# Performance work log

Hardware: AMD Instinct MI355X
Metric: run time of the kernel (lower is better)

Reference implementation:

```python
import jax, jax.numpy as jnp
import numpy as np

N = 100000      # nodes
D_IN = 512      # in_size
D_OUT = 512     # out_size
E = 200000      # edges per etype
EPS = 1e-5      # LayerNorm eps


def setup_inputs() -> dict:
    key = jax.random.key(0)
    ks = jax.random.split(key, 10)
    scale = 1.0 / np.sqrt(D_IN)
    inp = {
        "x": jax.random.normal(ks[0], (N, D_IN), jnp.float32),
        "W0": jax.random.normal(ks[1], (D_OUT, D_IN), jnp.float32) * scale,
        "W1": jax.random.normal(ks[2], (D_OUT, D_IN), jnp.float32) * scale,
        "W2": jax.random.normal(ks[3], (D_OUT, D_IN), jnp.float32) * scale,
        "gamma": jnp.ones((D_OUT,), jnp.float32),
        "beta": jnp.zeros((D_OUT,), jnp.float32),
        "src0": jax.random.randint(ks[4], (E,), 0, N, jnp.int32),
        "dst0": jax.random.randint(ks[5], (E,), 0, N, jnp.int32),
        "src1": jax.random.randint(ks[6], (E,), 0, N, jnp.int32),
        "dst1": jax.random.randint(ks[7], (E,), 0, N, jnp.int32),
        "src2": jax.random.randint(ks[8], (E,), 0, N, jnp.int32),
        "dst2": jax.random.randint(ks[9], (E,), 0, N, jnp.int32),
    }
    return inp


def _segment_mean(msgs, dst, n):
    # per-dst-node mean; 0 for nodes with no incoming edges (DGL fn.mean semantics)
    s = jax.ops.segment_sum(msgs, dst, num_segments=n)
    c = jax.ops.segment_sum(jnp.ones((msgs.shape[0],), msgs.dtype), dst, num_segments=n)
    return s / jnp.maximum(c, 1.0)[:, None]


def reference(x, W0, W1, W2, gamma, beta, src0, dst0, src1, dst1, src2, dst2):
    # relation-specific linear transforms, averaged over etypes sharing the src ntype
    h = (x @ W0.T + x @ W1.T + x @ W2.T) / 3.0            # [N, D_OUT]
    # per-etype copy_u / mean aggregation
    a0 = _segment_mean(h[src0], dst0, N)
    a1 = _segment_mean(h[src1], dst1, N)
    a2 = _segment_mean(h[src2], dst2, N)
    # cross-etype 'mean' reducer
    h_agg = (a0 + a1 + a2) / 3.0
    # LayerNorm(ReLU(h_agg))
    a = jax.nn.relu(h_agg)
    mu = jnp.mean(a, axis=-1, keepdims=True)
    var = jnp.mean(jnp.square(a - mu), axis=-1, keepdims=True)
    return (a - mu) * jax.lax.rsqrt(var + EPS) * gamma + beta
```

## Files before the change

### kernel.cpp

```cpp
#include <hip/hip_runtime.h>
#include <hip/hip_bf16.h>
#include <cstdint>
#include <cstddef>

#define N_NODES 100000
#define DIM 512
#define NE 200000
#define NBLK 391

typedef __attribute__((ext_vector_type(4))) float floatx4;
typedef __attribute__((ext_vector_type(8))) short shortx8;

__device__ __forceinline__ unsigned short f2bf(float f) {
    union { float f; uint32_t u; } v; v.f = f;
    uint32_t r = v.u + 0x7fff + ((v.u >> 16) & 1);
    return (unsigned short)(r >> 16);
}

__device__ __forceinline__ float bf2f(unsigned short h) {
    union { uint32_t u; float f; } v; v.u = ((uint32_t)h) << 16;
    return v.f;
}

__device__ __forceinline__ shortx8 cvt8(const float4 a, const float4 b) {
    union { __hip_bfloat162 h2[4]; shortx8 s8; } u;
    u.h2[0] = __float22bfloat162_rn(make_float2(a.x, a.y));
    u.h2[1] = __float22bfloat162_rn(make_float2(a.z, a.w));
    u.h2[2] = __float22bfloat162_rn(make_float2(b.x, b.y));
    u.h2[3] = __float22bfloat162_rn(make_float2(b.z, b.w));
    return u.s8;
}

__device__ __forceinline__ void load_lds16(const void* g, void* l) {
    __builtin_amdgcn_global_load_lds(
        (const __attribute__((address_space(1))) uint32_t*)g,
        (__attribute__((address_space(3))) uint32_t*)l, 16, 0, 0);
}

__global__ __launch_bounds__(256) void combine_w_kernel(
    const float* __restrict__ W0, const float* __restrict__ W1,
    const float* __restrict__ W2, unsigned short* __restrict__ Wc) {
    int i = blockIdx.x * 256 + threadIdx.x;
    Wc[i] = f2bf((W0[i] + W1[i] + W2[i]) * (1.0f / 3.0f));
}

__global__ __launch_bounds__(256) void count_kernel(
    const int* __restrict__ d0, const int* __restrict__ d1,
    const int* __restrict__ d2, int* __restrict__ cnt) {
    int t = blockIdx.x * 256 + threadIdx.x;
    if (t >= 3 * NE) return;
    int e = t / NE;
    int i = t - e * NE;
    const int* dp = (e == 0) ? d0 : (e == 1) ? d1 : d2;
    atomicAdd(&cnt[e * N_NODES + dp[i]], 1);
}

__global__ __launch_bounds__(256) void scan1_kernel(
    const int* __restrict__ cnt, int* __restrict__ bsum) {
    int t = threadIdx.x;
    int n = blockIdx.x * 256 + t;
    int rl = 0;
    if (n < N_NODES) rl = cnt[n] + cnt[N_NODES + n] + cnt[2 * N_NODES + n];
    int v = rl;
    #pragma unroll
    for (int off = 32; off > 0; off >>= 1) v += __shfl_xor(v, off);
    __shared__ int ws_[4];
    if ((t & 63) == 0) ws_[t >> 6] = v;
    __syncthreads();
    if (t == 0) bsum[blockIdx.x] = ws_[0] + ws_[1] + ws_[2] + ws_[3];
}

__global__ __launch_bounds__(512) void scan2_kernel(
    const int* __restrict__ bsum, int* __restrict__ boff) {
    __shared__ int sh[512];
    int t = threadIdx.x;
    int v = (t < NBLK) ? bsum[t] : 0;
    sh[t] = v;
    __syncthreads();
    #pragma unroll
    for (int off = 1; off < 512; off <<= 1) {
        int add = (t >= off) ? sh[t - off] : 0;
        __syncthreads();
        sh[t] += add;
        __syncthreads();
    }
    if (t < NBLK) boff[t] = sh[t] - v;
}

__global__ __launch_bounds__(256) void scan3_kernel(
    const int* __restrict__ cnt, const int* __restrict__ boff,
    int* __restrict__ row_start, int* __restrict__ cursor) {
    __shared__ int sh[256];
    int t = threadIdx.x;
    int n = blockIdx.x * 256 + t;
    int rl = 0;
    if (n < N_NODES) rl = cnt[n] + cnt[N_NODES + n] + cnt[2 * N_NODES + n];
    sh[t] = rl;
    __syncthreads();
    #pragma unroll
    for (int off = 1; off < 256; off <<= 1) {
        int add = (t >= off) ? sh[t - off] : 0;
        __syncthreads();
        sh[t] += add;
        __syncthreads();
    }
    if (n < N_NODES) {
        int excl = sh[t] - rl + boff[blockIdx.x];
        row_start[n] = excl;
        cursor[n] = excl;
    }
}

__global__ __launch_bounds__(256) void bin_kernel(
    const int* __restrict__ s0, const int* __restrict__ d0,
    const int* __restrict__ s1, const int* __restrict__ d1,
    const int* __restrict__ s2, const int* __restrict__ d2,
    int* __restrict__ cursor, int* __restrict__ src_tag) {
    int t = blockIdx.x * 256 + threadIdx.x;
    if (t >= 3 * NE) return;
    int e = t / NE;
    int i = t - e * NE;
    const int* sp; const int* dp;
    if (e == 0)      { sp = s0; dp = d0; }
    else if (e == 1) { sp = s1; dp = d1; }
    else             { sp = s2; dp = d2; }
    int d = dp[i];
    int pos = atomicAdd(&cursor[d], 1);
    src_tag[pos] = sp[i] | (e << 30);
}

__global__ __launch_bounds__(256) void gemm_kernel(
    const float* __restrict__ X, const unsigned short* __restrict__ B,
    unsigned short* __restrict__ H, int M) {
    __shared__ alignas(16) unsigned short As[128 * 64];
    __shared__ alignas(16) unsigned short Bs[128 * 64];
    const int tid = threadIdx.x;
    const int lane = tid & 63;
    const int w = tid >> 6;
    const int wr = w >> 1, wc = w & 1;
    const int q = lane >> 4, r = lane & 15;

    int lid = ((int)blockIdx.x & 7) * 391 + ((int)blockIdx.x >> 3);
    int mt = lid >> 2, nt = lid & 3;
    int m0 = mt * 128, n0 = nt * 128;

    const int arow = tid >> 3;
    const int ac = tid & 7;
    const int acs = ac ^ (arow & 7);
    const unsigned abyte = (unsigned)arow * 128 + (unsigned)acs * 16;
    const float* aptr[4];
    #pragma unroll
    for (int i = 0; i < 4; ++i) {
        int gm = m0 + i * 32 + arow; if (gm >= M) gm = M - 1;
        aptr[i] = X + (size_t)gm * DIM + ac * 8;
    }
    float4 areg[4][2];
    auto aload = [&](int k0_) {
        #pragma unroll
        for (int i = 0; i < 4; ++i) {
            areg[i][0] = *(const float4*)(aptr[i] + k0_);
            areg[i][1] = *(const float4*)(aptr[i] + k0_ + 4);
        }
    };

    floatx4 acc[4][4] = {};
    aload(0);

    for (int k0 = 0; k0 < DIM; k0 += 64) {
        #pragma unroll
        for (int i = 0; i < 4; ++i) {
            int ch = i * 256 + tid;
            int row = ch >> 3, c0 = ch & 7;
            int cs = c0 ^ (row & 7);
            load_lds16(&B[(size_t)(n0 + row) * DIM + k0 + cs * 8], &Bs[ch * 8]);
        }
        #pragma unroll
        for (int i = 0; i < 4; ++i)
            *(shortx8*)((char*)As + i * 4096 + abyte) = cvt8(areg[i][0], areg[i][1]);
        __syncthreads();
        if (k0 + 64 < DIM) aload(k0 + 64);

        #pragma unroll
        for (int kk = 0; kk < 2; ++kk) {
            const int kq = kk * 4 + q;
            const int sc = (kq ^ (r & 7)) * 16;
            shortx8 af[4], bfr[4];
            #pragma unroll
            for (int mi = 0; mi < 4; ++mi)
                af[mi] = *(const shortx8*)((const char*)As +
                         (wr * 64 + mi * 16 + r) * 128 + sc);
            #pragma unroll
            for (int nj = 0; nj < 4; ++nj)
                bfr[nj] = *(const shortx8*)((const char*)Bs +
                          (wc * 64 + nj * 16 + r) * 128 + sc);
            #pragma unroll
            for (int mi = 0; mi < 4; ++mi)
                #pragma unroll
                for (int nj = 0; nj < 4; ++nj)
                    acc[mi][nj] = __builtin_amdgcn_mfma_f32_16x16x32_bf16(
                        af[mi], bfr[nj], acc[mi][nj], 0, 0, 0);
        }
        __syncthreads();
    }

    #pragma unroll
    for (int mi = 0; mi < 4; ++mi) {
        #pragma unroll
        for (int rg = 0; rg < 4; ++rg) {
            int gm = m0 + wr * 64 + mi * 16 + q * 4 + rg;
            if (gm < M) {
                #pragma unroll
                for (int nj = 0; nj < 4; ++nj)
                    H[(size_t)gm * DIM + n0 + wc * 64 + nj * 16 + r] =
                        f2bf(acc[mi][nj][rg]);
            }
        }
    }
}

__global__ __launch_bounds__(256) void gather_ln_kernel(
    const unsigned short* __restrict__ h, const int* __restrict__ row_start,
    const int* __restrict__ cnt, const int* __restrict__ src_tag,
    const float* __restrict__ gamma, const float* __restrict__ beta,
    float* __restrict__ out) {
    const int lane = threadIdx.x & 63;
    const int n = blockIdx.x * 4 + (threadIdx.x >> 6);
    if (n >= N_NODES) return;
    const int c0 = cnt[n], c1 = cnt[N_NODES + n], c2 = cnt[2 * N_NODES + n];
    const int len = c0 + c1 + c2;
    const float w0 = 1.0f / (3.0f * (float)max(c0, 1));
    const float w1 = 1.0f / (3.0f * (float)max(c1, 1));
    const float w2 = 1.0f / (3.0f * (float)max(c2, 1));
    const int beg = row_start[n];
    const size_t lx = (size_t)lane * 8;
    float acc[8] = {};
    for (int base = 0; base < len; base += 64) {
        int rem = len - base;
        int m = rem < 64 ? rem : 64;
        int tag = (lane < m) ? src_tag[beg + base + lane] : 0;
        int j = 0;
        for (; j + 4 <= m; j += 4) {
            int u0 = __shfl(tag, j),     u1 = __shfl(tag, j + 1);
            int u2 = __shfl(tag, j + 2), u3 = __shfl(tag, j + 3);
            int e0 = ((unsigned)u0) >> 30, e1 = ((unsigned)u1) >> 30;
            int e2 = ((unsigned)u2) >> 30, e3 = ((unsigned)u3) >> 30;
            float g0 = (e0 == 0) ? w0 : ((e0 == 1) ? w1 : w2);
            float g1 = (e1 == 0) ? w0 : ((e1 == 1) ? w1 : w2);
            float g2 = (e2 == 0) ? w0 : ((e2 == 1) ? w1 : w2);
            float g3 = (e3 == 0) ? w0 : ((e3 == 1) ? w1 : w2);
            shortx8 v0 = *(const shortx8*)(h + (size_t)(u0 & 0x3FFFFFFF) * DIM + lx);
            shortx8 v1 = *(const shortx8*)(h + (size_t)(u1 & 0x3FFFFFFF) * DIM + lx);
            shortx8 v2 = *(const shortx8*)(h + (size_t)(u2 & 0x3FFFFFFF) * DIM + lx);
            shortx8 v3 = *(const shortx8*)(h + (size_t)(u3 & 0x3FFFFFFF) * DIM + lx);
            #pragma unroll
            for (int k = 0; k < 8; ++k) {
                acc[k] += bf2f((unsigned short)v0[k]) * g0;
                acc[k] += bf2f((unsigned short)v1[k]) * g1;
                acc[k] += bf2f((unsigned short)v2[k]) * g2;
                acc[k] += bf2f((unsigned short)v3[k]) * g3;
            }
        }
        for (; j < m; ++j) {
            int u = __shfl(tag, j);
            int e = ((unsigned)u) >> 30;
            float wg = (e == 0) ? w0 : ((e == 1) ? w1 : w2);
            shortx8 v = *(const shortx8*)(h + (size_t)(u & 0x3FFFFFFF) * DIM + lx);
            #pragma unroll
            for (int k = 0; k < 8; ++k)
                acc[k] += bf2f((unsigned short)v[k]) * wg;
        }
    }
    float s1_ = 0.0f, s2_ = 0.0f;
    #pragma unroll
    for (int k = 0; k < 8; ++k) {
        float v = fmaxf(acc[k], 0.0f);
        acc[k] = v; s1_ += v; s2_ += v * v;
    }
    #pragma unroll
    for (int off = 1; off < 64; off <<= 1) {
        s1_ += __shfl_xor(s1_, off);
        s2_ += __shfl_xor(s2_, off);
    }
    float mu = s1_ * (1.0f / DIM);
    float var = s2_ * (1.0f / DIM) - mu * mu;
    float rstd = rsqrtf(var + 1e-5f);
    float4 g0 = *(const float4*)(gamma + lane * 8);
    float4 g1 = *(const float4*)(gamma + lane * 8 + 4);
    float4 b0 = *(const float4*)(beta + lane * 8);
    float4 b1 = *(const float4*)(beta + lane * 8 + 4);
    float4 o0, o1;
    o0.x = (acc[0] - mu) * rstd * g0.x + b0.x;
    o0.y = (acc[1] - mu) * rstd * g0.y + b0.y;
    o0.z = (acc[2] - mu) * rstd * g0.z + b0.z;
    o0.w = (acc[3] - mu) * rstd * g0.w + b0.w;
    o1.x = (acc[4] - mu) * rstd * g1.x + b1.x;
    o1.y = (acc[5] - mu) * rstd * g1.y + b1.y;
    o1.z = (acc[6] - mu) * rstd * g1.z + b1.z;
    o1.w = (acc[7] - mu) * rstd * g1.w + b1.w;
    float4* op = (float4*)(out + (size_t)n * DIM + lane * 8);
    op[0] = o0;
    op[1] = o1;
}

extern "C" void kernel_launch(void* const* d_in, const int* in_sizes, int n_in,
                              void* d_out, int out_size, void* d_ws, size_t ws_size,
                              hipStream_t stream) {
    const float* x     = (const float*)d_in[0];
    const float* W0    = (const float*)d_in[1];
    const float* W1    = (const float*)d_in[2];
    const float* W2    = (const float*)d_in[3];
    const float* gamma = (const float*)d_in[4];
    const float* beta  = (const float*)d_in[5];
    const int* s0  = (const int*)d_in[6];
    const int* dd0 = (const int*)d_in[7];
    const int* s1  = (const int*)d_in[8];
    const int* dd1 = (const int*)d_in[9];
    const int* s2  = (const int*)d_in[10];
    const int* dd2 = (const int*)d_in[11];
    float* out = (float*)d_out;

    char* ws = (char*)d_ws;
    size_t off = 0;
    int* cnt = (int*)(ws + off);             off += 3u * N_NODES * 4u;
    int* row_start = (int*)(ws + off);       off += (size_t)N_NODES * 4u;
    int* cursor = (int*)(ws + off);          off += (size_t)N_NODES * 4u;
    int* bsum = (int*)(ws + off);            off += 2048;
    int* boff = (int*)(ws + off);            off += 2048;
    int* src_tag = (int*)(ws + off);         off += (size_t)3 * NE * 4u;
    unsigned short* Wc = (unsigned short*)(ws + off); off += (size_t)DIM * DIM * 2u;
    off = (off + 255) & ~255ull;
    unsigned short* h = (unsigned short*)(ws + off);

    hipMemsetAsync(cnt, 0, (size_t)3 * N_NODES * sizeof(int), stream);

    combine_w_kernel<<<(DIM * DIM) / 256, 256, 0, stream>>>(W0, W1, W2, Wc);
    count_kernel<<<(3 * NE + 255) / 256, 256, 0, stream>>>(dd0, dd1, dd2, cnt);
    scan1_kernel<<<NBLK, 256, 0, stream>>>(cnt, bsum);
    scan2_kernel<<<1, 512, 0, stream>>>(bsum, boff);
    scan3_kernel<<<NBLK, 256, 0, stream>>>(cnt, boff, row_start, cursor);
    bin_kernel<<<(3 * NE + 255) / 256, 256, 0, stream>>>(
        s0, dd0, s1, dd1, s2, dd2, cursor, src_tag);

    gemm_kernel<<<3128, 256, 0, stream>>>(x, Wc, h, N_NODES);

    gather_ln_kernel<<<(N_NODES + 3) / 4, 256, 0, stream>>>(
        h, row_start, cnt, src_tag, gamma, beta, out);
}
```

Before: 558.0 us.

## Double-buffer GEMM tiles, fuse preprocessing kernels, split gather rows across two waves

The GEMM now double-buffers its A and B LDS tiles and prefetches A two k-steps ahead. This lets global loads overlap the MFMA work at the cost of twice the shared memory. The weight-combine and edge-count kernels are merged into one launch, and the three-stage scan becomes two kernels with 512-thread blocks, with each block rescanning the block sums itself. The gather+LayerNorm kernel splits each node's 512 features across two waves with 4-element loads, adding an LDS reduction and a block barrier to raise memory parallelism.

```diff
diff --git a/kernel.cpp b/kernel.cpp
--- a/kernel.cpp
+++ b/kernel.cpp
@@ -6,10 +6,11 @@
 #define N_NODES 100000
 #define DIM 512
 #define NE 200000
-#define NBLK 391
+#define NSB 196
 
 typedef __attribute__((ext_vector_type(4))) float floatx4;
 typedef __attribute__((ext_vector_type(8))) short shortx8;
+typedef __attribute__((ext_vector_type(4))) short shortx4;
 
 __device__ __forceinline__ unsigned short f2bf(float f) {
     union { float f; uint32_t u; } v; v.f = f;
@@ -37,75 +38,72 @@
         (__attribute__((address_space(3))) uint32_t*)l, 16, 0, 0);
 }
 
-__global__ __launch_bounds__(256) void combine_w_kernel(
+__global__ __launch_bounds__(256) void count_combine_kernel(
+    const int* __restrict__ d0, const int* __restrict__ d1,
+    const int* __restrict__ d2, int* __restrict__ cnt,
     const float* __restrict__ W0, const float* __restrict__ W1,
     const float* __restrict__ W2, unsigned short* __restrict__ Wc) {
-    int i = blockIdx.x * 256 + threadIdx.x;
-    Wc[i] = f2bf((W0[i] + W1[i] + W2[i]) * (1.0f / 3.0f));
-}
-
-__global__ __launch_bounds__(256) void count_kernel(
-    const int* __restrict__ d0, const int* __restrict__ d1,
-    const int* __restrict__ d2, int* __restrict__ cnt) {
     int t = blockIdx.x * 256 + threadIdx.x;
-    if (t >= 3 * NE) return;
-    int e = t / NE;
-    int i = t - e * NE;
-    const int* dp = (e == 0) ? d0 : (e == 1) ? d1 : d2;
-    atomicAdd(&cnt[e * N_NODES + dp[i]], 1);
-}
-
-__global__ __launch_bounds__(256) void scan1_kernel(
+    if (t < DIM * DIM)
+        Wc[t] = f2bf((W0[t] + W1[t] + W2[t]) * (1.0f / 3.0f));
+    if (t < 3 * NE) {
+        int e = t / NE;
+        int i = t - e * NE;
+        const int* dp = (e == 0) ? d0 : (e == 1) ? d1 : d2;
+        atomicAdd(&cnt[e * N_NODES + dp[i]], 1);
+    }
+}
+
+__global__ __launch_bounds__(512) void scan1_kernel(
     const int* __restrict__ cnt, int* __restrict__ bsum) {
     int t = threadIdx.x;
-    int n = blockIdx.x * 256 + t;
+    int n = blockIdx.x * 512 + t;
     int rl = 0;
     if (n < N_NODES) rl = cnt[n] + cnt[N_NODES + n] + cnt[2 * N_NODES + n];
     int v = rl;
     #pragma unroll
     for (int off = 32; off > 0; off >>= 1) v += __shfl_xor(v, off);
-    __shared__ int ws_[4];
+    __shared__ int ws_[8];
     if ((t & 63) == 0) ws_[t >> 6] = v;
     __syncthreads();
-    if (t == 0) bsum[blockIdx.x] = ws_[0] + ws_[1] + ws_[2] + ws_[3];
-}
-
-__global__ __launch_bounds__(512) void scan2_kernel(
-    const int* __restrict__ bsum, int* __restrict__ boff) {
+    if (t == 0) {
+        int s = 0;
+        #pragma unroll
+        for (int i = 0; i < 8; ++i) s += ws_[i];
+        bsum[blockIdx.x] = s;
+    }
+}
+
+__global__ __launch_bounds__(512) void scan3_kernel(
+    const int* __restrict__ cnt, const int* __restrict__ bsum,
+    int* __restrict__ row_start, int* __restrict__ cursor) {
+    __shared__ int shb[512];
     __shared__ int sh[512];
     int t = threadIdx.x;
-    int v = (t < NBLK) ? bsum[t] : 0;
-    sh[t] = v;
+    shb[t] = (t < NSB) ? bsum[t] : 0;
     __syncthreads();
     #pragma unroll
     for (int off = 1; off < 512; off <<= 1) {
-        int add = (t >= off) ? sh[t - off] : 0;
-        __syncthreads();
-        sh[t] += add;
-        __syncthreads();
-    }
-    if (t < NBLK) boff[t] = sh[t] - v;
-}
-
-__global__ __launch_bounds__(256) void scan3_kernel(
-    const int* __restrict__ cnt, const int* __restrict__ boff,
-    int* __restrict__ row_start, int* __restrict__ cursor) {
-    __shared__ int sh[256];
-    int t = threadIdx.x;
-    int n = blockIdx.x * 256 + t;
+        int add = (t >= off) ? shb[t - off] : 0;
+        __syncthreads();
+        shb[t] += add;
+        __syncthreads();
+    }
+    int n = blockIdx.x * 512 + t;
     int rl = 0;
     if (n < N_NODES) rl = cnt[n] + cnt[N_NODES + n] + cnt[2 * N_NODES + n];
     sh[t] = rl;
     __syncthreads();
     #pragma unroll
-    for (int off = 1; off < 256; off <<= 1) {
+    for (int off = 1; off < 512; off <<= 1) {
         int add = (t >= off) ? sh[t - off] : 0;
         __syncthreads();
         sh[t] += add;
         __syncthreads();
     }
     if (n < N_NODES) {
-        int excl = sh[t] - rl + boff[blockIdx.x];
+        int bexcl = shb[blockIdx.x] - bsum[blockIdx.x];
+        int excl = sh[t] - rl + bexcl;
         row_start[n] = excl;
         cursor[n] = excl;
     }
@@ -132,8 +130,8 @@
 __global__ __launch_bounds__(256) void gemm_kernel(
     const float* __restrict__ X, const unsigned short* __restrict__ B,
     unsigned short* __restrict__ H, int M) {
-    __shared__ alignas(16) unsigned short As[128 * 64];
-    __shared__ alignas(16) unsigned short Bs[128 * 64];
+    __shared__ alignas(16) unsigned short As[2][128 * 64];
+    __shared__ alignas(16) unsigned short Bs[2][128 * 64];
     const int tid = threadIdx.x;
     const int lane = tid & 63;
     const int w = tid >> 6;
@@ -154,32 +152,48 @@
         int gm = m0 + i * 32 + arow; if (gm >= M) gm = M - 1;
         aptr[i] = X + (size_t)gm * DIM + ac * 8;
     }
-    float4 areg[4][2];
-    auto aload = [&](int k0_) {
+
+    float4 areg[2][4][2];
+    auto aload = [&](int p, int k0_) {
         #pragma unroll
         for (int i = 0; i < 4; ++i) {
-            areg[i][0] = *(const float4*)(aptr[i] + k0_);
-            areg[i][1] = *(const float4*)(aptr[i] + k0_ + 4);
+            areg[p][i][0] = *(const float4*)(aptr[i] + k0_);
+            areg[p][i][1] = *(const float4*)(aptr[i] + k0_ + 4);
         }
     };
-
-    floatx4 acc[4][4] = {};
-    aload(0);
-
-    for (int k0 = 0; k0 < DIM; k0 += 64) {
+    auto writeA = [&](int buf, int p) {
+        #pragma unroll
+        for (int i = 0; i < 4; ++i)
+            *(shortx8*)((char*)As[buf] + i * 4096 + abyte) =
+                cvt8(areg[p][i][0], areg[p][i][1]);
+    };
+    auto stageB = [&](int buf, int k0_) {
         #pragma unroll
         for (int i = 0; i < 4; ++i) {
             int ch = i * 256 + tid;
-            int row = ch >> 3, c0 = ch & 7;
-            int cs = c0 ^ (row & 7);
-            load_lds16(&B[(size_t)(n0 + row) * DIM + k0 + cs * 8], &Bs[ch * 8]);
-        }
-        #pragma unroll
-        for (int i = 0; i < 4; ++i)
-            *(shortx8*)((char*)As + i * 4096 + abyte) = cvt8(areg[i][0], areg[i][1]);
-        __syncthreads();
-        if (k0 + 64 < DIM) aload(k0 + 64);
-
+            int row = ch >> 3, c0_ = ch & 7;
+            int cs = c0_ ^ (row & 7);
+            load_lds16(&B[(size_t)(n0 + row) * DIM + k0_ + cs * 8], &Bs[buf][ch * 8]);
+        }
+    };
+
+    floatx4 acc[4][4] = {};
+
+    aload(0, 0);
+    stageB(0, 0);
+    writeA(0, 0);
+    aload(1, 64);
+    aload(0, 128);
+    __syncthreads();
+
+    #pragma unroll
+    for (int t = 0; t < 8; ++t) {
+        const int cur = t & 1;
+        if (t < 7) {
+            stageB(cur ^ 1, (t + 1) * 64);
+            writeA(cur ^ 1, (t + 1) & 1);
+            if (t < 5) aload((t + 1) & 1, (t + 3) * 64);
+        }
         #pragma unroll
         for (int kk = 0; kk < 2; ++kk) {
             const int kq = kk * 4 + q;
@@ -187,11 +201,11 @@
             shortx8 af[4], bfr[4];
             #pragma unroll
             for (int mi = 0; mi < 4; ++mi)
-                af[mi] = *(const shortx8*)((const char*)As +
+                af[mi] = *(const shortx8*)((const char*)As[cur] +
                          (wr * 64 + mi * 16 + r) * 128 + sc);
             #pragma unroll
             for (int nj = 0; nj < 4; ++nj)
-                bfr[nj] = *(const shortx8*)((const char*)Bs +
+                bfr[nj] = *(const shortx8*)((const char*)Bs[cur] +
                           (wc * 64 + nj * 16 + r) * 128 + sc);
             #pragma unroll
             for (int mi = 0; mi < 4; ++mi)
@@ -223,83 +237,89 @@
     const int* __restrict__ cnt, const int* __restrict__ src_tag,
     const float* __restrict__ gamma, const float* __restrict__ beta,
     float* __restrict__ out) {
-    const int lane = threadIdx.x & 63;
-    const int n = blockIdx.x * 4 + (threadIdx.x >> 6);
-    if (n >= N_NODES) return;
-    const int c0 = cnt[n], c1 = cnt[N_NODES + n], c2 = cnt[2 * N_NODES + n];
-    const int len = c0 + c1 + c2;
-    const float w0 = 1.0f / (3.0f * (float)max(c0, 1));
-    const float w1 = 1.0f / (3.0f * (float)max(c1, 1));
-    const float w2 = 1.0f / (3.0f * (float)max(c2, 1));
-    const int beg = row_start[n];
-    const size_t lx = (size_t)lane * 8;
-    float acc[8] = {};
-    for (int base = 0; base < len; base += 64) {
-        int rem = len - base;
-        int m = rem < 64 ? rem : 64;
-        int tag = (lane < m) ? src_tag[beg + base + lane] : 0;
-        int j = 0;
-        for (; j + 4 <= m; j += 4) {
-            int u0 = __shfl(tag, j),     u1 = __shfl(tag, j + 1);
-            int u2 = __shfl(tag, j + 2), u3 = __shfl(tag, j + 3);
-            int e0 = ((unsigned)u0) >> 30, e1 = ((unsigned)u1) >> 30;
-            int e2 = ((unsigned)u2) >> 30, e3 = ((unsigned)u3) >> 30;
-            float g0 = (e0 == 0) ? w0 : ((e0 == 1) ? w1 : w2);
-            float g1 = (e1 == 0) ? w0 : ((e1 == 1) ? w1 : w2);
-            float g2 = (e2 == 0) ? w0 : ((e2 == 1) ? w1 : w2);
-            float g3 = (e3 == 0) ? w0 : ((e3 == 1) ? w1 : w2);
-            shortx8 v0 = *(const shortx8*)(h + (size_t)(u0 & 0x3FFFFFFF) * DIM + lx);
-            shortx8 v1 = *(const shortx8*)(h + (size_t)(u1 & 0x3FFFFFFF) * DIM + lx);
-            shortx8 v2 = *(const shortx8*)(h + (size_t)(u2 & 0x3FFFFFFF) * DIM + lx);
-            shortx8 v3 = *(const shortx8*)(h + (size_t)(u3 & 0x3FFFFFFF) * DIM + lx);
-            #pragma unroll
-            for (int k = 0; k < 8; ++k) {
-                acc[k] += bf2f((unsigned short)v0[k]) * g0;
-                acc[k] += bf2f((unsigned short)v1[k]) * g1;
-                acc[k] += bf2f((unsigned short)v2[k]) * g2;
-                acc[k] += bf2f((unsigned short)v3[k]) * g3;
+    const int tid = threadIdx.x;
+    const int lane = tid & 63;
+    const int half = (tid >> 6) & 1;
+    const int nloc = tid >> 7;
+    const int n = blockIdx.x * 2 + nloc;
+    __shared__ float red[2][2][2];
+    const bool alive = (n < N_NODES);
+
+    int len = 0, beg = 0;
+    float w0 = 0.0f, w1 = 0.0f, w2 = 0.0f;
+    if (alive) {
+        int c0 = cnt[n], c1 = cnt[N_NODES + n], c2 = cnt[2 * N_NODES + n];
+        len = c0 + c1 + c2;
+        w0 = 1.0f / (3.0f * (float)max(c0, 1));
+        w1 = 1.0f / (3.0f * (float)max(c1, 1));
+        w2 = 1.0f / (3.0f * (float)max(c2, 1));
+        beg = row_start[n];
+    }
+    const int d0 = half * 256 + lane * 4;
+    float acc[4] = {};
+    if (alive) {
+        for (int base = 0; base < len; base += 64) {
+            int rem = len - base;
+            int m = rem < 64 ? rem : 64;
+            int tag = (lane < m) ? src_tag[beg + base + lane] : 0;
+            int j = 0;
+            for (; j + 4 <= m; j += 4) {
+                int u0 = __shfl(tag, j),     u1 = __shfl(tag, j + 1);
+                int u2 = __shfl(tag, j + 2), u3 = __shfl(tag, j + 3);
+                float g0 = (((unsigned)u0 >> 30) == 0) ? w0 : ((((unsigned)u0 >> 30) == 1) ? w1 : w2);
+                float g1 = (((unsigned)u1 >> 30) == 0) ? w0 : ((((unsigned)u1 >> 30) == 1) ? w1 : w2);
+                float g2 = (((unsigned)u2 >> 30) == 0) ? w0 : ((((unsigned)u2 >> 30) == 1) ? w1 : w2);
+                float g3 = (((unsigned)u3 >> 30) == 0) ? w0 : ((((unsigned)u3 >> 30) == 1) ? w1 : w2);
+                shortx4 v0 = *(const shortx4*)(h + (size_t)(u0 & 0x3FFFFFFF) * DIM + d0);
+                shortx4 v1 = *(const shortx4*)(h + (size_t)(u1 & 0x3FFFFFFF) * DIM + d0);
+                shortx4 v2 = *(const shortx4*)(h + (size_t)(u2 & 0x3FFFFFFF) * DIM + d0);
+                shortx4 v3 = *(const shortx4*)(h + (size_t)(u3 & 0x3FFFFFFF) * DIM + d0);
+                #pragma unroll
+                for (int k = 0; k < 4; ++k) {
+                    acc[k] += bf2f((unsigned short)v0[k]) * g0;
+                    acc[k] += bf2f((unsigned short)v1[k]) * g1;
+                    acc[k] += bf2f((unsigned short)v2[k]) * g2;
+                    acc[k] += bf2f((unsigned short)v3[k]) * g3;
+                }
             }
-        }
-        for (; j < m; ++j) {
-            int u = __shfl(tag, j);
-            int e = ((unsigned)u) >> 30;
-            float wg = (e == 0) ? w0 : ((e == 1) ? w1 : w2);
-            shortx8 v = *(const shortx8*)(h + (size_t)(u & 0x3FFFFFFF) * DIM + lx);
-            #pragma unroll
-            for (int k = 0; k < 8; ++k)
-                acc[k] += bf2f((unsigned short)v[k]) * wg;
-        }
-    }
-    float s1_ = 0.0f, s2_ = 0.0f;
-    #pragma unroll
-    for (int k = 0; k < 8; ++k) {
+            for (; j < m; ++j) {
+                int u = __shfl(tag, j);
+                float wg = (((unsigned)u >> 30) == 0) ? w0 : ((((unsigned)u >> 30) == 1) ? w1 : w2);
+                shortx4 v = *(const shortx4*)(h + (size_t)(u & 0x3FFFFFFF) * DIM + d0);
+                #pragma unroll
+                for (int k = 0; k < 4; ++k)
+                    acc[k] += bf2f((unsigned short)v[k]) * wg;
+            }
+        }
+    }
+    float s1 = 0.0f, s2 = 0.0f;
+    #pragma unroll
+    for (int k = 0; k < 4; ++k) {
         float v = fmaxf(acc[k], 0.0f);
-        acc[k] = v; s1_ += v; s2_ += v * v;
+        acc[k] = v; s1 += v; s2 += v * v;
     }
     #pragma unroll
     for (int off = 1; off < 64; off <<= 1) {
-        s1_ += __shfl_xor(s1_, off);
-        s2_ += __shfl_xor(s2_, off);
-    }
-    float mu = s1_ * (1.0f / DIM);
-    float var = s2_ * (1.0f / DIM) - mu * mu;
-    float rstd = rsqrtf(var + 1e-5f);
-    float4 g0 = *(const float4*)(gamma + lane * 8);
-    float4 g1 = *(const float4*)(gamma + lane * 8 + 4);
-    float4 b0 = *(const float4*)(beta + lane * 8);
-    float4 b1 = *(const float4*)(beta + lane * 8 + 4);
-    float4 o0, o1;
-    o0.x = (acc[0] - mu) * rstd * g0.x + b0.x;
-    o0.y = (acc[1] - mu) * rstd * g0.y + b0.y;
-    o0.z = (acc[2] - mu) * rstd * g0.z + b0.z;
-    o0.w = (acc[3] - mu) * rstd * g0.w + b0.w;
-    o1.x = (acc[4] - mu) * rstd * g1.x + b1.x;
-    o1.y = (acc[5] - mu) * rstd * g1.y + b1.y;
-    o1.z = (acc[6] - mu) * rstd * g1.z + b1.z;
-    o1.w = (acc[7] - mu) * rstd * g1.w + b1.w;
-    float4* op = (float4*)(out + (size_t)n * DIM + lane * 8);
-    op[0] = o0;
-    op[1] = o1;
+        s1 += __shfl_xor(s1, off);
+        s2 += __shfl_xor(s2, off);
+    }
+    if (lane == 0) { red[nloc][half][0] = s1; red[nloc][half][1] = s2; }
+    __syncthreads();
+    float S1 = red[nloc][0][0] + red[nloc][1][0];
+    float S2 = red[nloc][0][1] + red[nloc][1][1];
+    if (alive) {
+        float mu = S1 * (1.0f / DIM);
+        float var = S2 * (1.0f / DIM) - mu * mu;
+        float rstd = rsqrtf(var + 1e-5f);
+        float4 g = *(const float4*)(gamma + d0);
+        float4 b = *(const float4*)(beta + d0);
+        float4 o;
+        o.x = (acc[0] - mu) * rstd * g.x + b.x;
+        o.y = (acc[1] - mu) * rstd * g.y + b.y;
+        o.z = (acc[2] - mu) * rstd * g.z + b.z;
+        o.w = (acc[3] - mu) * rstd * g.w + b.w;
+        *(float4*)(out + (size_t)n * DIM + d0) = o;
+    }
 }
 
 extern "C" void kernel_launch(void* const* d_in, const int* in_sizes, int n_in,
@@ -325,7 +345,6 @@
     int* row_start = (int*)(ws + off);       off += (size_t)N_NODES * 4u;
     int* cursor = (int*)(ws + off);          off += (size_t)N_NODES * 4u;
     int* bsum = (int*)(ws + off);            off += 2048;
-    int* boff = (int*)(ws + off);            off += 2048;
     int* src_tag = (int*)(ws + off);         off += (size_t)3 * NE * 4u;
     unsigned short* Wc = (unsigned short*)(ws + off); off += (size_t)DIM * DIM * 2u;
     off = (off + 255) & ~255ull;
@@ -333,16 +352,15 @@
 
     hipMemsetAsync(cnt, 0, (size_t)3 * N_NODES * sizeof(int), stream);
 
-    combine_w_kernel<<<(DIM * DIM) / 256, 256, 0, stream>>>(W0, W1, W2, Wc);
-    count_kernel<<<(3 * NE + 255) / 256, 256, 0, stream>>>(dd0, dd1, dd2, cnt);
-    scan1_kernel<<<NBLK, 256, 0, stream>>>(cnt, bsum);
-    scan2_kernel<<<1, 512, 0, stream>>>(bsum, boff);
-    scan3_kernel<<<NBLK, 256, 0, stream>>>(cnt, boff, row_start, cursor);
+    count_combine_kernel<<<(3 * NE + 255) / 256, 256, 0, stream>>>(
+        dd0, dd1, dd2, cnt, W0, W1, W2, Wc);
+    scan1_kernel<<<NSB, 512, 0, stream>>>(cnt, bsum);
+    scan3_kernel<<<NSB, 512, 0, stream>>>(cnt, bsum, row_start, cursor);
     bin_kernel<<<(3 * NE + 255) / 256, 256, 0, stream>>>(
         s0, dd0, s1, dd1, s2, dd2, cursor, src_tag);
 
     gemm_kernel<<<3128, 256, 0, stream>>>(x, Wc, h, N_NODES);
 
-    gather_ln_kernel<<<(N_NODES + 3) / 4, 256, 0, stream>>>(
+    gather_ln_kernel<<<(N_NODES + 1) / 2, 256, 0, stream>>>(
         h, row_start, cnt, src_tag, gamma, beta, out);
 }
```

New measurement: 592.1 us. 6.1% more time.
